# Performance work log

Measured on AMD Instinct MI355X. Metric: run time of the kernel, lower is better.

Reference implementation:

```python
import jax, jax.numpy as jnp
import numpy as np

N_NODES = 50000
N_EDGES = 800000
K = 15          # kernel points
P_DIM = 3
IN_DIM = 32
OUT_DIM = 64
KP_EXTENT = 0.6


def setup_inputs() -> dict:
    key = jax.random.key(0)
    k1, k2, k3, k4, k5, k6 = jax.random.split(key, 6)
    pos = jax.random.normal(k1, (N_NODES, P_DIM), dtype=jnp.float32)
    feat = jax.random.normal(k2, (N_NODES, IN_DIM), dtype=jnp.float32)
    # kernel point layout inside a ball of the given radius (load_kernels stand-in)
    kernel_points = jax.random.normal(k3, (K, P_DIM), dtype=jnp.float32) * 0.5
    kernel_points = kernel_points.at[0].set(0.0)  # fixed center point
    weights = jax.random.normal(k4, (K, IN_DIM, OUT_DIM), dtype=jnp.float32) * (1.0 / np.sqrt(IN_DIM))
    edge_src = jax.random.randint(k5, (N_EDGES,), 0, N_NODES, dtype=jnp.int32)
    edge_dst = jax.random.randint(k6, (N_EDGES,), 0, N_NODES, dtype=jnp.int32)
    return {"pos": pos, "feat": feat, "kernel_points": kernel_points,
            "weights": weights, "edge_src": edge_src, "edge_dst": edge_dst}


def reference(pos, feat, kernel_points, weights, edge_src, edge_dst):
    n_nodes = pos.shape[0]
    # per-edge relative position: src - dst  [E, p]
    y = pos[edge_src] - pos[edge_dst]
    # distance to each kernel point  [E, k]
    diff = y[:, None, :] - kernel_points[None, :, :]
    dist = jnp.sqrt(jnp.sum(diff * diff, axis=-1))
    # linear correlation influence  [E, k]
    m = jax.nn.relu(1.0 - dist / KP_EXTENT)
    # per-edge weighted features  [E, k, in]
    f = feat[edge_src]
    contrib = m[:, :, None] * f[:, None, :]
    # segment-reduce onto destination nodes  [N, k, in]
    weighted_f = jax.ops.segment_sum(contrib, edge_dst, num_segments=n_nodes)
    # per-kernel-point matmul and sum over kernel points  [N, out]
    return jnp.einsum('nki,kio->no', weighted_f, weights)
```

## Files before the change

kernel.cpp:

```cpp
#include <hip/hip_runtime.h>
#include <hip/hip_fp16.h>

#define N_NODES 50000
#define N_EDGES 800000
#define KPTS 15
#define IN_DIM 32
#define OUT_DIM 64
#define KP_EXTENT 0.6f
#define INV_EXT (1.0f / KP_EXTENT)
#define EXT2 (KP_EXTENT * KP_EXTENT)

#define CAP 131072
#define NREP 16
#define SEG_CAP (CAP / NREP)
#define CNT_STRIDE 32
#define K1_BLOCKS (N_EDGES / 256)
#define SUBB 4
#define WPS (SUBB * 4)

#define PCNT_OFF 32768
#define WH_OFF   262144
#define FEATH_OFF (1u << 20)
#define LIST_OFF  (8u << 20)
#define SLOT_OFF  (32u << 20)
#define SCAP_MAX 16

typedef unsigned int uint;
typedef _Float16 f16x8 __attribute__((ext_vector_type(8)));
typedef float f32x4 __attribute__((ext_vector_type(4)));

union FU { uint u[4]; f16x8 h; };
union HU { unsigned short us; _Float16 h; };

static __device__ __forceinline__ float h2f16(uint u) {
    return __half2float(__ushort_as_half((unsigned short)(u & 0xffffu)));
}
static __device__ __forceinline__ uint pack2(float lo, float hi) {
    return (uint)__half_as_ushort(__float2half_rn(lo))
         | ((uint)__half_as_ushort(__float2half_rn(hi)) << 16);
}

__global__ __launch_bounds__(256) void geom_compact(
    const float* __restrict__ pos,
    const float* __restrict__ feat,
    const float* __restrict__ kp,
    const float* __restrict__ W,
    const int*   __restrict__ esrc,
    const int*   __restrict__ edst,
    int*         __restrict__ cnt,
    int*         __restrict__ pcnt,
    uint2*       __restrict__ lists,
    uint*        __restrict__ featH,
    uint*        __restrict__ WH,
    float4*      __restrict__ outz,
    uint*        __restrict__ slots16,
    const int scap)
{
    __shared__ int s_wavecnt[KPTS][4];
    __shared__ int s_woff[KPTS][4];
    __shared__ int s_base[KPTS];

    const int tid  = threadIdx.x;
    const int wv   = tid >> 6;
    const int lane = tid & 63;
    const int rep  = blockIdx.x & (NREP - 1);

    const int e = blockIdx.x * 256 + tid;

    outz[e] = make_float4(0.0f, 0.0f, 0.0f, 0.0f);
    {
        const float2 fv = ((const float2*)feat)[e];
        featH[e] = pack2(fv.x, fv.y);
    }
    if (e < KPTS * (IN_DIM / 2) * OUT_DIM) {
        const int c  = e & 63;
        const int f0 = 2 * e - c;
        WH[e] = pack2(W[f0], W[f0 + 64]);
    }

    const int s = esrc[e];
    const int d = edst[e];

    const float yx = pos[s * 3 + 0] - pos[d * 3 + 0];
    const float yy = pos[s * 3 + 1] - pos[d * 3 + 1];
    const float yz = pos[s * 3 + 2] - pos[d * 3 + 2];

    float d2v[KPTS];
    unsigned act = 0;
    #pragma unroll
    for (int k = 0; k < KPTS; ++k) {
        const float dx = yx - kp[k * 3 + 0];
        const float dy = yy - kp[k * 3 + 1];
        const float dz = yz - kp[k * 3 + 2];
        const float d2 = dx * dx + dy * dy + dz * dz;
        d2v[k] = d2;
        if (d2 < EXT2) act |= (1u << k);
    }

    const int nact = __popc(act);
    int ti = 0;
    if (nact > 0) ti = atomicAdd(pcnt + d, nact);

    unsigned long long kmask[KPTS];
    #pragma unroll
    for (int k = 0; k < KPTS; ++k) {
        kmask[k] = __ballot((act >> k) & 1u);
        if (lane == 0) s_wavecnt[k][wv] = __popcll(kmask[k]);
    }
    __syncthreads();

    if (tid < KPTS) {
        int o0 = 0;
        #pragma unroll
        for (int w = 0; w < 4; ++w) {
            s_woff[tid][w] = o0;
            o0 += s_wavecnt[tid][w];
        }
        s_base[tid] = (o0 > 0)
            ? atomicAdd(&cnt[(tid * NREP + rep) * CNT_STRIDE], o0) : 0;
    }
    __syncthreads();

    const unsigned long long lt = (lane == 63) ? 0x7fffffffffffffffull
                                               : ((1ull << lane) - 1ull);
    #pragma unroll
    for (int k = 0; k < KPTS; ++k) {
        const unsigned long long mask = kmask[k];
        if (mask == 0ull) continue;
        if ((act >> k) & 1u) {
            const int rank = __popcll(mask & lt);
            const int idx  = s_base[k] + s_woff[k][wv] + rank;

            const int t = ti;
            ++ti;
            const unsigned ey = (t < scap)
                ? (unsigned)((d * scap + t) * OUT_DIM)
                : (0x80000000u | (unsigned)d);

            if (idx < SEG_CAP) {
                const float mk = 1.0f - sqrtf(d2v[k]) * INV_EXT;
                const unsigned mh =
                    (unsigned)__half_as_ushort(__float2half(mk));
                lists[(size_t)k * CAP + (size_t)rep * SEG_CAP + idx] =
                    make_uint2(((unsigned)s << 16) | mh, ey);
            } else if (!(ey & 0x80000000u)) {
                uint* row = slots16 + (ey >> 1);
                #pragma unroll
                for (int j = 0; j < OUT_DIM / 2; ++j) row[j] = 0u;
            }
        }
    }
}

__global__ __launch_bounds__(256) void pair_matmul(
    const uint*  __restrict__ featH,
    const uint*  __restrict__ WH,
    const int*   __restrict__ cnt,
    const uint2* __restrict__ lists,
    float*       __restrict__ out,
    uint*        __restrict__ slots16)
{
    const int seg  = blockIdx.x % (KPTS * NREP);
    const int sub  = blockIdx.x / (KPTS * NREP);
    const int k    = seg >> 4;
    const int rep  = seg & (NREP - 1);
    const int wv   = threadIdx.x >> 6;
    const int lane = threadIdx.x & 63;
    const int col  = lane & 15;
    const int grp  = lane >> 4;

    uint bu[4][4];
    const uint* __restrict__ Whk = WH + k * 1024 + grp * 256 + col;
    #pragma unroll
    for (int t = 0; t < 4; ++t)
        #pragma unroll
        for (int j = 0; j < 4; ++j)
            bu[t][j] = Whk[j * 64 + t * 16];
    #pragma unroll
    for (int t = 0; t < 4; ++t)
        #pragma unroll
        for (int j = 0; j < 4; ++j)
            asm volatile("" : "+v"(bu[t][j]));

    int n = cnt[seg * CNT_STRIDE];
    if (n > SEG_CAP) n = SEG_CAP;
    const uint2* __restrict__ list =
        lists + (size_t)k * CAP + (size_t)rep * SEG_CAP;
    const int nsteps = (n + 15) >> 4;

    int s = sub * 4 + wv;
    if (s >= nsteps) return;

    uint2 ent;
    {
        const int pi = s * 16 + col;
        ent = (pi < n) ? list[pi] : make_uint2(0u, 0xFFFFFFFFu);
    }
    FU A;
    {
        const uint* __restrict__ fp = featH + (ent.x >> 16) * 16 + grp * 4;
        #pragma unroll
        for (int j = 0; j < 4; ++j) A.u[j] = fp[j];
    }

    while (true) {
        const int s2 = s + WPS;
        uint2 entN = make_uint2(0u, 0xFFFFFFFFu);
        if (s2 < nsteps) {
            const int pi2 = s2 * 16 + col;
            if (pi2 < n) entN = list[pi2];
        }

        HU mu; mu.us = (unsigned short)(ent.x & 0xffffu);
        const f16x8 ms = {mu.h, mu.h, mu.h, mu.h, mu.h, mu.h, mu.h, mu.h};
        FU As; As.h = A.h * ms;

        f32x4 C0 = {0,0,0,0}, C1 = {0,0,0,0}, C2 = {0,0,0,0}, C3 = {0,0,0,0};
        {
            FU b0, b1, b2, b3;
            #pragma unroll
            for (int j = 0; j < 4; ++j) {
                b0.u[j] = bu[0][j]; b1.u[j] = bu[1][j];
                b2.u[j] = bu[2][j]; b3.u[j] = bu[3][j];
            }
            C0 = __builtin_amdgcn_mfma_f32_16x16x32_f16(As.h, b0.h, C0, 0, 0, 0);
            C1 = __builtin_amdgcn_mfma_f32_16x16x32_f16(As.h, b1.h, C1, 0, 0, 0);
            C2 = __builtin_amdgcn_mfma_f32_16x16x32_f16(As.h, b2.h, C2, 0, 0, 0);
            C3 = __builtin_amdgcn_mfma_f32_16x16x32_f16(As.h, b3.h, C3, 0, 0, 0);
        }

        #pragma unroll
        for (int i = 0; i < 4; ++i) {
            const int r = grp * 4 + i;
            const uint er = (uint)__shfl((int)ent.y, r);
            if (er == 0xFFFFFFFFu) continue;
            if (!(er & 0x80000000u)) {
                __half* __restrict__ sp = (__half*)slots16 + (size_t)er + col;
                sp[0]  = __float2half_rn(C0[i]);
                sp[16] = __float2half_rn(C1[i]);
                sp[32] = __float2half_rn(C2[i]);
                sp[48] = __float2half_rn(C3[i]);
            } else {
                float* __restrict__ op = out + (size_t)(er & 0xffffu) * OUT_DIM + col;
                atomicAdd(op +  0, C0[i]);
                atomicAdd(op + 16, C1[i]);
                atomicAdd(op + 32, C2[i]);
                atomicAdd(op + 48, C3[i]);
            }
        }

        if (s2 >= nsteps) break;
        s = s2;
        ent = entN;
        const uint* __restrict__ fp = featH + (ent.x >> 16) * 16 + grp * 4;
        #pragma unroll
        for (int j = 0; j < 4; ++j) A.u[j] = fp[j];
    }
}

__global__ __launch_bounds__(256) void node_reduce(
    const int*  __restrict__ pcnt,
    const uint* __restrict__ slots16,
    float*      __restrict__ out,
    const int scap)
{
    const int wv   = threadIdx.x >> 6;
    const int lane = threadIdx.x & 63;
    const int node = blockIdx.x * 8 + wv * 2 + (lane >> 5);
    const int l    = lane & 31;

    const int raw = pcnt[node];
    int deg = raw;
    if (deg > scap) deg = scap;

    const uint* __restrict__ sp =
        slots16 + (size_t)node * ((size_t)scap * 32) + l;

    float a0 = 0.0f, a1 = 0.0f, b0 = 0.0f, b1 = 0.0f;
    int j = 0;
    for (; j + 1 < deg; j += 2) {
        const uint u0 = sp[(size_t)j * 32];
        const uint u1 = sp[(size_t)(j + 1) * 32];
        a0 += h2f16(u0); a1 += h2f16(u0 >> 16);
        b0 += h2f16(u1); b1 += h2f16(u1 >> 16);
    }
    if (j < deg) {
        const uint u0 = sp[(size_t)j * 32];
        a0 += h2f16(u0); a1 += h2f16(u0 >> 16);
    }

    float o0 = a0 + b0;
    float o1 = a1 + b1;
    if (raw > scap) {
        const float2 prev = ((const float2*)out)[(size_t)node * 32 + l];
        o0 += prev.x; o1 += prev.y;
    }
    ((float2*)out)[(size_t)node * 32 + l] = make_float2(o0, o1);
}

extern "C" void kernel_launch(void* const* d_in, const int* in_sizes, int n_in,
                              void* d_out, int out_size, void* d_ws, size_t ws_size,
                              hipStream_t stream)
{
    const float* pos  = (const float*)d_in[0];
    const float* feat = (const float*)d_in[1];
    const float* kp   = (const float*)d_in[2];
    const float* W    = (const float*)d_in[3];
    const int* esrc   = (const int*)d_in[4];
    const int* edst   = (const int*)d_in[5];
    float* out        = (float*)d_out;

    int*   cnt     = (int*)d_ws;
    int*   pcnt    = (int*)((char*)d_ws + PCNT_OFF);
    uint*  WH      = (uint*)((char*)d_ws + WH_OFF);
    uint*  featH   = (uint*)((char*)d_ws + FEATH_OFF);
    uint2* lists   = (uint2*)((char*)d_ws + LIST_OFF);
    uint*  slots16 = (uint*)((char*)d_ws + SLOT_OFF);

    const size_t layer_bytes = (size_t)N_NODES * OUT_DIM * 2;
    int scap = 0;
    if (ws_size >= (size_t)SLOT_OFF + layer_bytes) {
        scap = (int)((ws_size - (size_t)SLOT_OFF) / layer_bytes);
        if (scap > SCAP_MAX) scap = SCAP_MAX;
    }

    hipMemsetAsync(d_ws, 0, 262144, stream);

    geom_compact<<<K1_BLOCKS, 256, 0, stream>>>(pos, feat, kp, W, esrc, edst,
                                                cnt, pcnt, lists, featH, WH,
                                                (float4*)out, slots16, scap);
    pair_matmul<<<SUBB * KPTS * NREP, 256, 0, stream>>>(featH, WH, cnt, lists,
                                                        out, slots16);
    if (scap > 0)
        node_reduce<<<N_NODES / 8, 256, 0, stream>>>(pcnt, slots16, out, scap);
}
```

Baseline: 113.8 us.

## Fuse three-kernel pipeline into one cooperative persistent kernel with grid syncs

Replaces the memset plus three separate launches with a single cooperative kernel. A persistent grid strides over the zeroing/conversion, edge geometry compaction, MFMA pair matmul and node-reduce phases, separated by grid.sync(). The aim is to remove the launch overhead and inter-kernel gaps. In exchange the grid is capped at occupancy times CU count, so each block processes many tiles serially, and the grid-wide barriers add their own cost. The old multi-kernel path is kept as a fallback.

```diff
diff --git a/kernel.cpp b/kernel.cpp
--- a/kernel.cpp
+++ b/kernel.cpp
@@ -1,5 +1,8 @@
 #include <hip/hip_runtime.h>
 #include <hip/hip_fp16.h>
+#include <hip/hip_cooperative_groups.h>
+
+namespace cg = cooperative_groups;
 
 #define N_NODES 50000
 #define N_EDGES 800000
@@ -14,9 +17,10 @@
 #define NREP 16
 #define SEG_CAP (CAP / NREP)
 #define CNT_STRIDE 32
-#define K1_BLOCKS (N_EDGES / 256)
+#define K1_TILES (N_EDGES / 256)
 #define SUBB 4
 #define WPS (SUBB * 4)
+#define MAX_GRID 1024
 
 #define PCNT_OFF 32768
 #define WH_OFF   262144
@@ -38,6 +42,271 @@
 static __device__ __forceinline__ uint pack2(float lo, float hi) {
     return (uint)__half_as_ushort(__float2half_rn(lo))
          | ((uint)__half_as_ushort(__float2half_rn(hi)) << 16);
+}
+
+__global__ __launch_bounds__(256) void kpconv_fused(
+    const float* __restrict__ pos,
+    const float* __restrict__ feat,
+    const float* __restrict__ kp,
+    const float* __restrict__ W,
+    const int*   __restrict__ esrc,
+    const int*   __restrict__ edst,
+    int*         __restrict__ cnt,
+    int*         __restrict__ pcnt,
+    uint2*       __restrict__ lists,
+    uint*        __restrict__ featH,
+    uint*        __restrict__ WH,
+    float*       __restrict__ out,
+    uint*        __restrict__ slots16,
+    const int scap)
+{
+    cg::grid_group grid = cg::this_grid();
+
+    __shared__ int s_wavecnt[KPTS][4];
+    __shared__ int s_woff[KPTS][4];
+    __shared__ int s_base[KPTS];
+
+    const int tid  = threadIdx.x;
+    const int wv   = tid >> 6;
+    const int lane = tid & 63;
+    const int nb   = gridDim.x;
+    const int gid  = blockIdx.x * 256 + tid;
+    const int gsz  = nb * 256;
+
+    {
+        float4* outz = (float4*)out;
+        for (int i = gid; i < N_EDGES; i += gsz) {
+            outz[i] = make_float4(0.0f, 0.0f, 0.0f, 0.0f);
+            const float2 fv = ((const float2*)feat)[i];
+            featH[i] = pack2(fv.x, fv.y);
+        }
+        for (int i = gid; i < N_NODES; i += gsz) pcnt[i] = 0;
+        if (gid < KPTS * NREP) cnt[gid * CNT_STRIDE] = 0;
+        if (gid < KPTS * (IN_DIM / 2) * OUT_DIM) {
+            const int c  = gid & 63;
+            const int f0 = 2 * gid - c;
+            WH[gid] = pack2(W[f0], W[f0 + 64]);
+        }
+    }
+    grid.sync();
+
+    for (int tile = blockIdx.x; tile < K1_TILES; tile += nb) {
+        const int rep = tile & (NREP - 1);
+        const int e   = tile * 256 + tid;
+
+        const int s = esrc[e];
+        const int d = edst[e];
+
+        const float yx = pos[s * 3 + 0] - pos[d * 3 + 0];
+        const float yy = pos[s * 3 + 1] - pos[d * 3 + 1];
+        const float yz = pos[s * 3 + 2] - pos[d * 3 + 2];
+
+        float d2v[KPTS];
+        unsigned act = 0;
+        #pragma unroll
+        for (int k = 0; k < KPTS; ++k) {
+            const float dx = yx - kp[k * 3 + 0];
+            const float dy = yy - kp[k * 3 + 1];
+            const float dz = yz - kp[k * 3 + 2];
+            const float d2 = dx * dx + dy * dy + dz * dz;
+            d2v[k] = d2;
+            if (d2 < EXT2) act |= (1u << k);
+        }
+
+        const int nact = __popc(act);
+        int ti = 0;
+        if (nact > 0) ti = atomicAdd(pcnt + d, nact);
+
+        unsigned long long kmask[KPTS];
+        #pragma unroll
+        for (int k = 0; k < KPTS; ++k) {
+            kmask[k] = __ballot((act >> k) & 1u);
+            if (lane == 0) s_wavecnt[k][wv] = __popcll(kmask[k]);
+        }
+        __syncthreads();
+
+        if (tid < KPTS) {
+            int o0 = 0;
+            #pragma unroll
+            for (int w = 0; w < 4; ++w) {
+                s_woff[tid][w] = o0;
+                o0 += s_wavecnt[tid][w];
+            }
+            s_base[tid] = (o0 > 0)
+                ? atomicAdd(&cnt[(tid * NREP + rep) * CNT_STRIDE], o0) : 0;
+        }
+        __syncthreads();
+
+        const unsigned long long lt = (lane == 63) ? 0x7fffffffffffffffull
+                                                   : ((1ull << lane) - 1ull);
+        #pragma unroll
+        for (int k = 0; k < KPTS; ++k) {
+            const unsigned long long mask = kmask[k];
+            if (mask == 0ull) continue;
+            if ((act >> k) & 1u) {
+                const int rank = __popcll(mask & lt);
+                const int idx  = s_base[k] + s_woff[k][wv] + rank;
+
+                const int t = ti;
+                ++ti;
+                const unsigned ey = (t < scap)
+                    ? (unsigned)((d * scap + t) * OUT_DIM)
+                    : (0x80000000u | (unsigned)d);
+
+                if (idx < SEG_CAP) {
+                    const float mk = 1.0f - sqrtf(d2v[k]) * INV_EXT;
+                    const unsigned mh =
+                        (unsigned)__half_as_ushort(__float2half(mk));
+                    lists[(size_t)k * CAP + (size_t)rep * SEG_CAP + idx] =
+                        make_uint2(((unsigned)s << 16) | mh, ey);
+                } else if (!(ey & 0x80000000u)) {
+                    uint* row = slots16 + (ey >> 1);
+                    #pragma unroll
+                    for (int j = 0; j < OUT_DIM / 2; ++j) row[j] = 0u;
+                }
+            }
+        }
+        __syncthreads();
+    }
+    grid.sync();
+
+    for (int sb = blockIdx.x; sb < KPTS * NREP * SUBB; sb += nb) {
+        const int seg = sb % (KPTS * NREP);
+        const int sub = sb / (KPTS * NREP);
+        const int k   = seg >> 4;
+        const int rep = seg & (NREP - 1);
+        const int col = lane & 15;
+        const int grp = lane >> 4;
+
+        uint bu[4][4];
+        const uint* __restrict__ Whk = WH + k * 1024 + grp * 256 + col;
+        #pragma unroll
+        for (int t = 0; t < 4; ++t)
+            #pragma unroll
+            for (int j = 0; j < 4; ++j)
+                bu[t][j] = Whk[j * 64 + t * 16];
+        #pragma unroll
+        for (int t = 0; t < 4; ++t)
+            #pragma unroll
+            for (int j = 0; j < 4; ++j)
+                asm volatile("" : "+v"(bu[t][j]));
+
+        int n = cnt[seg * CNT_STRIDE];
+        if (n > SEG_CAP) n = SEG_CAP;
+        const uint2* __restrict__ list =
+            lists + (size_t)k * CAP + (size_t)rep * SEG_CAP;
+        const int nsteps = (n + 15) >> 4;
+
+        int s = sub * 4 + wv;
+        if (s < nsteps) {
+            uint2 ent;
+            {
+                const int pi = s * 16 + col;
+                ent = (pi < n) ? list[pi] : make_uint2(0u, 0xFFFFFFFFu);
+            }
+            FU A;
+            {
+                const uint* __restrict__ fp =
+                    featH + (ent.x >> 16) * 16 + grp * 4;
+                #pragma unroll
+                for (int j = 0; j < 4; ++j) A.u[j] = fp[j];
+            }
+
+            while (true) {
+                const int s2 = s + WPS;
+                uint2 entN = make_uint2(0u, 0xFFFFFFFFu);
+                if (s2 < nsteps) {
+                    const int pi2 = s2 * 16 + col;
+                    if (pi2 < n) entN = list[pi2];
+                }
+
+                HU mu; mu.us = (unsigned short)(ent.x & 0xffffu);
+                const f16x8 ms = {mu.h, mu.h, mu.h, mu.h,
+                                  mu.h, mu.h, mu.h, mu.h};
+                FU As; As.h = A.h * ms;
+
+                f32x4 C0 = {0,0,0,0}, C1 = {0,0,0,0},
+                      C2 = {0,0,0,0}, C3 = {0,0,0,0};
+                {
+                    FU b0, b1, b2, b3;
+                    #pragma unroll
+                    for (int j = 0; j < 4; ++j) {
+                        b0.u[j] = bu[0][j]; b1.u[j] = bu[1][j];
+                        b2.u[j] = bu[2][j]; b3.u[j] = bu[3][j];
+                    }
+                    C0 = __builtin_amdgcn_mfma_f32_16x16x32_f16(As.h, b0.h, C0, 0, 0, 0);
+                    C1 = __builtin_amdgcn_mfma_f32_16x16x32_f16(As.h, b1.h, C1, 0, 0, 0);
+                    C2 = __builtin_amdgcn_mfma_f32_16x16x32_f16(As.h, b2.h, C2, 0, 0, 0);
+                    C3 = __builtin_amdgcn_mfma_f32_16x16x32_f16(As.h, b3.h, C3, 0, 0, 0);
+                }
+
+                #pragma unroll
+                for (int i = 0; i < 4; ++i) {
+                    const int r = grp * 4 + i;
+                    const uint er = (uint)__shfl((int)ent.y, r);
+                    if (er == 0xFFFFFFFFu) continue;
+                    if (!(er & 0x80000000u)) {
+                        __half* __restrict__ sp =
+                            (__half*)slots16 + (size_t)er + col;
+                        sp[0]  = __float2half_rn(C0[i]);
+                        sp[16] = __float2half_rn(C1[i]);
+                        sp[32] = __float2half_rn(C2[i]);
+                        sp[48] = __float2half_rn(C3[i]);
+                    } else {
+                        float* __restrict__ op =
+                            out + (size_t)(er & 0xffffu) * OUT_DIM + col;
+                        atomicAdd(op +  0, C0[i]);
+                        atomicAdd(op + 16, C1[i]);
+                        atomicAdd(op + 32, C2[i]);
+                        atomicAdd(op + 48, C3[i]);
+                    }
+                }
+
+                if (s2 >= nsteps) break;
+                s = s2;
+                ent = entN;
+                const uint* __restrict__ fp =
+                    featH + (ent.x >> 16) * 16 + grp * 4;
+                #pragma unroll
+                for (int j = 0; j < 4; ++j) A.u[j] = fp[j];
+            }
+        }
+    }
+    grid.sync();
+
+    for (int nbase = blockIdx.x * 8; nbase < N_NODES; nbase += nb * 8) {
+        const int node = nbase + wv * 2 + (lane >> 5);
+        if (node >= N_NODES) continue;
+        const int l = lane & 31;
+
+        const int raw = pcnt[node];
+        int deg = raw;
+        if (deg > scap) deg = scap;
+
+        const uint* __restrict__ sp =
+            slots16 + (size_t)node * ((size_t)scap * 32) + l;
+
+        float a0 = 0.0f, a1 = 0.0f, b0 = 0.0f, b1 = 0.0f;
+        int j = 0;
+        for (; j + 1 < deg; j += 2) {
+            const uint u0 = sp[(size_t)j * 32];
+            const uint u1 = sp[(size_t)(j + 1) * 32];
+            a0 += h2f16(u0); a1 += h2f16(u0 >> 16);
+            b0 += h2f16(u1); b1 += h2f16(u1 >> 16);
+        }
+        if (j < deg) {
+            const uint u0 = sp[(size_t)j * 32];
+            a0 += h2f16(u0); a1 += h2f16(u0 >> 16);
+        }
+
+        float o0 = a0 + b0;
+        float o1 = a1 + b1;
+        if (raw > scap) {
+            const float2 prev = ((const float2*)out)[(size_t)node * 32 + l];
+            o0 += prev.x; o1 += prev.y;
+        }
+        ((float2*)out)[(size_t)node * 32 + l] = make_float2(o0, o1);
+    }
 }
 
 __global__ __launch_bounds__(256) void geom_compact(
@@ -324,11 +593,45 @@
         if (scap > SCAP_MAX) scap = SCAP_MAX;
     }
 
+    static int fused_grid = -2;
+    if (fused_grid == -2) {
+        int coop = 0, mab = 0, ncu = 0;
+        if (hipDeviceGetAttribute(&coop, hipDeviceAttributeCooperativeLaunch, 0)
+            != hipSuccess) coop = 0;
+        if (coop &&
+            hipOccupancyMaxActiveBlocksPerMultiprocessor(&mab, kpconv_fused,
+                                                         256, 0) == hipSuccess &&
+            hipDeviceGetAttribute(&ncu,
+                hipDeviceAttributeMultiprocessorCount, 0) == hipSuccess &&
+            mab > 0 && ncu > 0) {
+            int g = mab * ncu;
+            if (g > MAX_GRID) g = MAX_GRID;
+            fused_grid = g;
+        } else {
+            fused_grid = -1;
+        }
+    }
+
+    if (fused_grid > 0 && scap > 0) {
+        void* args[] = {
+            (void*)&pos, (void*)&feat, (void*)&kp, (void*)&W,
+            (void*)&esrc, (void*)&edst,
+            (void*)&cnt, (void*)&pcnt, (void*)&lists,
+            (void*)&featH, (void*)&WH,
+            (void*)&out, (void*)&slots16, (void*)&scap
+        };
+        hipError_t err = hipLaunchCooperativeKernel(
+            kpconv_fused, dim3(fused_grid), dim3(256), args, 0, stream);
+        if (err == hipSuccess) return;
+        (void)hipGetLastError();
+        fused_grid = -1;
+    }
+
     hipMemsetAsync(d_ws, 0, 262144, stream);
 
-    geom_compact<<<K1_BLOCKS, 256, 0, stream>>>(pos, feat, kp, W, esrc, edst,
-                                                cnt, pcnt, lists, featH, WH,
-                                                (float4*)out, slots16, scap);
+    geom_compact<<<K1_TILES, 256, 0, stream>>>(pos, feat, kp, W, esrc, edst,
+                                               cnt, pcnt, lists, featH, WH,
+                                               (float4*)out, slots16, scap);
     pair_matmul<<<SUBB * KPTS * NREP, 256, 0, stream>>>(featH, WH, cnt, lists,
                                                         out, slots16);
     if (scap > 0)
```

Measured after the change: 393.4 us. 246% more time.
